# Kernel optimization log

Measured on AMD Instinct MI355X. Metric: run time of the kernel, lower is better.

The kernel has to match this reference:

```python
import jax, jax.numpy as jnp
import numpy as np

B, S, D, H = 2, 2048, 1024, 16
DK = D // H
SOFTCAP = 30.0


def setup_inputs() -> dict:
    key = jax.random.key(0)
    ks = jax.random.split(key, 6)
    inp = jax.random.normal(ks[0], (B, S, D), dtype=jnp.float32)
    count_bias = jax.random.normal(ks[1], (B, 1, S, S), dtype=jnp.float32) * 0.1
    # causal boolean mask: True = allowed
    causal = jnp.tril(jnp.ones((S, S), dtype=bool))
    attn_mask = jnp.broadcast_to(causal[None, None, :, :], (B, 1, S, S))
    scale = 0.02
    Wq = jax.random.normal(ks[2], (D, D), dtype=jnp.float32) * scale
    Wk = jax.random.normal(ks[3], (D, D), dtype=jnp.float32) * scale
    Wv = jax.random.normal(ks[4], (D, D), dtype=jnp.float32) * scale
    Wo = jax.random.normal(ks[5], (D, D), dtype=jnp.float32) * scale
    return {"inp": inp, "count_bias": count_bias, "attn_mask": attn_mask,
            "Wq": Wq, "Wk": Wk, "Wv": Wv, "Wo": Wo}


def reference(inp, count_bias, attn_mask, Wq, Wk, Wv, Wo):
    b = inp.shape[0]
    # nn.Linear: y = x @ W.T ; reshape to (B, H, S, DK)
    def proj(x, W):
        return jnp.einsum('bsd,ed->bse', x, W).reshape(b, -1, H, DK).transpose(0, 2, 1, 3)
    q = proj(inp, Wq)
    k = proj(inp, Wk)
    v = proj(inp, Wv)
    scale = 1.0 / np.sqrt(DK).astype(np.float32)
    scores = jnp.einsum('bhqd,bhkd->bhqk', q, k) * scale  # (B,H,S,S)
    scores = scores + count_bias  # broadcast over heads
    scores = jnp.tanh(scores / SOFTCAP) * SOFTCAP  # softcap > 0
    scores = jnp.where(attn_mask, scores, -jnp.inf)
    weights = jax.nn.softmax(scores, axis=-1)
    o = jnp.einsum('bhqk,bhkd->bhqd', weights, v)
    o = o.transpose(0, 2, 1, 3).reshape(b, -1, D)
    out = jnp.einsum('bsd,ed->bse', o, Wo)
    return out
```

## Files before the change

### kernel.cpp

```cpp
#include <hip/hip_runtime.h>
#include <hip/hip_bf16.h>

#define GK 1024

typedef __attribute__((ext_vector_type(8))) short bf16x8;
typedef __attribute__((ext_vector_type(4))) float f32x4;
typedef __attribute__((ext_vector_type(16))) float f32x16;
typedef __attribute__((ext_vector_type(4))) unsigned short ushort4v;

__device__ __forceinline__ f32x4 mfma16(bf16x8 a, bf16x8 b, f32x4 c) {
  return __builtin_amdgcn_mfma_f32_16x16x32_bf16(a, b, c, 0, 0, 0);
}
__device__ __forceinline__ f32x16 mfma32(bf16x8 a, bf16x8 b, f32x16 c) {
  return __builtin_amdgcn_mfma_f32_32x32x16_bf16(a, b, c, 0, 0, 0);
}

__device__ __forceinline__ unsigned short f2b(float f) {
  union { float f; unsigned int u; } x; x.f = f;
  return (unsigned short)((x.u + 0x7fffu + ((x.u >> 16) & 1u)) >> 16);
}

__device__ __forceinline__ unsigned int pk2(float lo, float hi) {
  float2 f; f.x = lo; f.y = hi;
  __hip_bfloat162 t = __float22bfloat162_rn(f);
  union { __hip_bfloat162 b; unsigned int u; } c; c.b = t;
  return c.u;
}

__device__ __forceinline__ float fexp2(float x) {
#if __has_builtin(__builtin_amdgcn_exp2f)
  return __builtin_amdgcn_exp2f(x);
#else
  return exp2f(x);
#endif
}
__device__ __forceinline__ float frcp(float x) {
#if __has_builtin(__builtin_amdgcn_rcpf)
  return __builtin_amdgcn_rcpf(x);
#else
  return 1.0f / x;
#endif
}

__device__ __forceinline__ void gl_lds16(const unsigned short* g, unsigned short* l) {
  __builtin_amdgcn_global_load_lds(
      (const __attribute__((address_space(1))) unsigned int*)g,
      (__attribute__((address_space(3))) unsigned int*)l, 16, 0, 0);
}

__global__ __launch_bounds__(256) void convert_kernel(
    const float* __restrict__ inp,
    const float* __restrict__ wq, const float* __restrict__ wk,
    const float* __restrict__ wv, const float* __restrict__ wo,
    unsigned short* __restrict__ Xb, unsigned short* __restrict__ Wcat)
{
  const size_t XN = (size_t)4194304;
  size_t i = ((size_t)blockIdx.x * 256 + threadIdx.x) * 4;
  const float* src; unsigned short* dst; size_t off;
  if (i < XN) {
    src = inp; dst = Xb; off = i;
  } else {
    size_t j = i - XN;
    int w = (int)(j >> 20);
    off = j & 1048575u;
    src = (w == 0) ? wq : (w == 1) ? wk : (w == 2) ? wv : wo;
    dst = Wcat + ((size_t)w << 20);
  }
  f32x4 v = *(const f32x4*)(src + off);
  ushort4v o;
#pragma unroll
  for (int t = 0; t < 4; ++t) o[t] = f2b(v[t]);
  *(ushort4v*)(dst + off) = o;
}

__device__ __forceinline__ void gemm_mainloop(
    const unsigned short* __restrict__ A, const unsigned short* __restrict__ Wt,
    int m0, int n0, int tid, unsigned short* As, unsigned short* Bs,
    f32x4 (&acc)[4][4])
{
  const int lane = tid & 63;
  const int wave = tid >> 6;
  const int wr = wave >> 1, wc = wave & 1;
  const int lq = lane & 15, g = lane >> 4;

  const int r_in = lane >> 2;
  const int c8 = (lane & 3) * 8;

  const unsigned short* Ap0 = A + (size_t)(m0 + wave * 32 + r_in) * GK + c8;
  const unsigned short* Ap1 = Ap0 + (size_t)16 * GK;
  const unsigned short* Wp0 = Wt + (size_t)(n0 + wave * 32 + r_in) * GK + c8;
  const unsigned short* Wp1 = Wp0 + (size_t)16 * GK;
  unsigned short* As0 = As + wave * 1024;
  unsigned short* Bs0 = Bs + wave * 1024;

  for (int kt = 0; kt < GK / 32; ++kt) {
    const int k0 = kt * 32;
    __syncthreads();
    gl_lds16(Ap0 + k0, As0);
    gl_lds16(Ap1 + k0, As0 + 512);
    gl_lds16(Wp0 + k0, Bs0);
    gl_lds16(Wp1 + k0, Bs0 + 512);
    __syncthreads();
    bf16x8 af[4], bfr[4];
#pragma unroll
    for (int i = 0; i < 4; ++i)
      af[i] = *(const bf16x8*)(As + (wr * 64 + i * 16 + lq) * 32 + g * 8);
#pragma unroll
    for (int j = 0; j < 4; ++j)
      bfr[j] = *(const bf16x8*)(Bs + (wc * 64 + j * 16 + lq) * 32 + g * 8);
#pragma unroll
    for (int i = 0; i < 4; ++i)
#pragma unroll
      for (int j = 0; j < 4; ++j)
        acc[i][j] = mfma16(af[i], bfr[j], acc[i][j]);
  }
}

__global__ __launch_bounds__(256) void gemm_qkv(
    const unsigned short* __restrict__ X, const unsigned short* __restrict__ Wcat,
    unsigned short* __restrict__ Qb, unsigned short* __restrict__ Kb,
    unsigned short* __restrict__ Vt)
{
  __shared__ unsigned short As[4096];
  __shared__ unsigned short Bs[4096];
  f32x4 acc[4][4];
#pragma unroll
  for (int i = 0; i < 4; ++i)
#pragma unroll
    for (int j = 0; j < 4; ++j) acc[i][j] = (f32x4){0.f, 0.f, 0.f, 0.f};

  const int z = blockIdx.z;
  const int m0 = blockIdx.x * 128, n0 = blockIdx.y * 128;
  gemm_mainloop(X, Wcat + ((size_t)z << 20), m0, n0, (int)threadIdx.x, As, Bs, acc);

  const int lane = threadIdx.x & 63;
  const int wave = threadIdx.x >> 6;
  const int wr = wave >> 1, wc = wave & 1, lq = lane & 15, g = lane >> 4;

  if (z < 2) {
    unsigned short* C = z ? Kb : Qb;
#pragma unroll
    for (int i = 0; i < 4; ++i)
#pragma unroll
      for (int j = 0; j < 4; ++j) {
        int col = n0 + wc * 64 + j * 16 + lq;
#pragma unroll
        for (int r = 0; r < 4; ++r) {
          int row = m0 + wr * 64 + i * 16 + g * 4 + r;
          C[(size_t)row * 1024 + col] = f2b(acc[i][j][r]);
        }
      }
  } else {
#pragma unroll
    for (int i = 0; i < 4; ++i)
#pragma unroll
      for (int j = 0; j < 4; ++j) {
        int col = n0 + wc * 64 + j * 16 + lq;
        int row0 = m0 + wr * 64 + i * 16 + g * 4;
        int b = row0 >> 11;
        int s = row0 & 2047;
        ushort4v pv;
#pragma unroll
        for (int r = 0; r < 4; ++r) pv[r] = f2b(acc[i][j][r]);
        *(ushort4v*)(Vt + (size_t)(b * 1024 + col) * 2048 + s) = pv;
      }
  }
}

__global__ __launch_bounds__(256) void gemm_out(
    const unsigned short* __restrict__ Ob, const unsigned short* __restrict__ Wo,
    float* __restrict__ out)
{
  __shared__ unsigned short As[4096];
  __shared__ unsigned short Bs[4096];
  f32x4 acc[4][4];
#pragma unroll
  for (int i = 0; i < 4; ++i)
#pragma unroll
    for (int j = 0; j < 4; ++j) acc[i][j] = (f32x4){0.f, 0.f, 0.f, 0.f};

  const int m0 = blockIdx.x * 128, n0 = blockIdx.y * 128;
  gemm_mainloop(Ob, Wo, m0, n0, (int)threadIdx.x, As, Bs, acc);

  const int lane = threadIdx.x & 63;
  const int wave = threadIdx.x >> 6;
  const int wr = wave >> 1, wc = wave & 1, lq = lane & 15, g = lane >> 4;
#pragma unroll
  for (int i = 0; i < 4; ++i)
#pragma unroll
    for (int j = 0; j < 4; ++j) {
      int col = n0 + wc * 64 + j * 16 + lq;
#pragma unroll
      for (int r = 0; r < 4; ++r) {
        int row = m0 + wr * 64 + i * 16 + g * 4 + r;
        out[(size_t)row * 1024 + col] = acc[i][j][r];
      }
    }
}

__device__ __forceinline__ void attn_chain(
    const bf16x8 (&qf)[4], const f32x4 (&bvs)[4],
    bf16x8 kf0, bf16x8 kf1, bf16x8 kf2, bf16x8 kf3,
    bf16x8 va00, bf16x8 va01, bf16x8 va10, bf16x8 va11,
    bool msk, int ql, int hi,
    f32x16& o0, f32x16& o1, float& pls)
{
  const float INV30 = 0.033333333333f;
  const float C3 = -0.333333333f, C5 = 0.133333333f;
  const float C1 = 43.28085122666891f;

  f32x16 st = {0.f,0.f,0.f,0.f,0.f,0.f,0.f,0.f,0.f,0.f,0.f,0.f,0.f,0.f,0.f,0.f};
  st = mfma32(kf0, qf[0], st);
  st = mfma32(kf1, qf[1], st);
  st = mfma32(kf2, qf[2], st);
  st = mfma32(kf3, qf[3], st);

  float p[16];
#pragma unroll
  for (int reg = 0; reg < 16; ++reg) {
    float v = fmaf(st[reg], 0.125f, bvs[reg >> 2][reg & 3]);
    float y = v * INV30;
    float y2 = y * y;
    float t = y * fmaf(y2, fmaf(y2, C5, C3), 1.0f);
    p[reg] = fexp2(fmaf(t, C1, -C1));
  }
  if (msk) {
#pragma unroll
    for (int reg = 0; reg < 16; ++reg) {
      int krow = (reg & 3) + 8 * (reg >> 2) + 4 * hi;
      p[reg] = (krow <= ql) ? p[reg] : 0.f;
    }
  }
  float a0 = (p[0] + p[1]) + (p[2] + p[3]);
  float a1 = (p[4] + p[5]) + (p[6] + p[7]);
  float a2 = (p[8] + p[9]) + (p[10] + p[11]);
  float a3 = (p[12] + p[13]) + (p[14] + p[15]);
  pls += (a0 + a1) + (a2 + a3);

  unsigned int wv[8];
#pragma unroll
  for (int j = 0; j < 8; ++j) wv[j] = pk2(p[2 * j], p[2 * j + 1]);
  unsigned int x0 = hi ? wv[0] : wv[2], x1 = hi ? wv[1] : wv[3];
  x0 = __shfl_xor(x0, 32); x1 = __shfl_xor(x1, 32);
  unsigned int y0 = hi ? wv[4] : wv[6], y1 = hi ? wv[5] : wv[7];
  y0 = __shfl_xor(y0, 32); y1 = __shfl_xor(y1, 32);
  union { unsigned int u[4]; bf16x8 v; } B0, B1;
  B0.u[0] = hi ? x0 : wv[0]; B0.u[1] = hi ? x1 : wv[1];
  B0.u[2] = hi ? wv[2] : x0; B0.u[3] = hi ? wv[3] : x1;
  B1.u[0] = hi ? y0 : wv[4]; B1.u[1] = hi ? y1 : wv[5];
  B1.u[2] = hi ? wv[6] : y0; B1.u[3] = hi ? wv[7] : y1;

  o0 = mfma32(va00, B0.v, o0);
  o0 = mfma32(va01, B1.v, o0);
  o1 = mfma32(va10, B0.v, o1);
  o1 = mfma32(va11, B1.v, o1);
}

__global__ __launch_bounds__(256, 2) void attn_fwd(
    const unsigned short* __restrict__ Qb, const unsigned short* __restrict__ Kb,
    const unsigned short* __restrict__ Vt, const float* __restrict__ bias,
    unsigned short* __restrict__ Ob)
{
  __shared__ float Obuf[2][2][64 * 33];
  __shared__ float lsumbuf[2][8 * 32];
  __shared__ float rowinv[2][32];

  const int lane = threadIdx.x & 63;
  const int w = threadIdx.x >> 6;
  const int bid = blockIdx.x;
  const int lwg = (bid & 7) * 128 + (bid >> 3);
  const int bh = lwg >> 5;
  const int qp = lwg & 31;
  const int b = bh >> 4, h = bh & 15;
  const int tA = qp, tB = 63 - qp;
  const int q0A = tA * 32, q0B = tB * 32;
  const int ql = lane & 31;
  const int hi = lane >> 5;

  const unsigned short* QpA = Qb + (size_t)(b * 2048 + q0A + ql) * 1024 + h * 64 + 8 * hi;
  const unsigned short* QpB = Qb + (size_t)(b * 2048 + q0B + ql) * 1024 + h * 64 + 8 * hi;
  bf16x8 qfA[4], qfB[4];
#pragma unroll
  for (int c = 0; c < 4; ++c) {
    qfA[c] = *(const bf16x8*)(QpA + 16 * c);
    qfB[c] = *(const bf16x8*)(QpB + 16 * c);
  }

  const unsigned short* Kp = Kb + (size_t)(b * 2048 + ql) * 1024 + h * 64 + 8 * hi;
  const unsigned short* Vp = Vt + (size_t)(bh * 64 + ql) * 2048 + 8 * hi;
  const float* BpA = bias + (size_t)b * 4194304 + (size_t)(q0A + ql) * 2048 + 4 * hi;
  const float* BpB = bias + (size_t)b * 4194304 + (size_t)(q0B + ql) * 2048 + 4 * hi;

  float plsA = 0.f, plsB = 0.f;
  f32x16 oA0 = {0.f,0.f,0.f,0.f,0.f,0.f,0.f,0.f,0.f,0.f,0.f,0.f,0.f,0.f,0.f,0.f};
  f32x16 oA1 = oA0, oB0 = oA0, oB1 = oA0;

  for (int kt = w; kt <= tB; kt += 4) {
    const int k0 = kt * 32;
    const unsigned short* kp = Kp + (size_t)k0 * 1024;
    bf16x8 kf0 = *(const bf16x8*)(kp);
    bf16x8 kf1 = *(const bf16x8*)(kp + 16);
    bf16x8 kf2 = *(const bf16x8*)(kp + 32);
    bf16x8 kf3 = *(const bf16x8*)(kp + 48);
    const unsigned short* vp = Vp + k0;
    bf16x8 va00 = *(const bf16x8*)(vp);
    bf16x8 va01 = *(const bf16x8*)(vp + 16);
    bf16x8 va10 = *(const bf16x8*)(vp + (size_t)32 * 2048);
    bf16x8 va11 = *(const bf16x8*)(vp + (size_t)32 * 2048 + 16);
    f32x4 bvsB[4];
#pragma unroll
    for (int j = 0; j < 4; ++j) bvsB[j] = *(const f32x4*)(BpB + k0 + 8 * j);
    if (kt <= tA) {
      f32x4 bvsA[4];
#pragma unroll
      for (int j = 0; j < 4; ++j) bvsA[j] = *(const f32x4*)(BpA + k0 + 8 * j);
      attn_chain(qfA, bvsA, kf0, kf1, kf2, kf3, va00, va01, va10, va11,
                 kt == tA, ql, hi, oA0, oA1, plsA);
    }
    attn_chain(qfB, bvsB, kf0, kf1, kf2, kf3, va00, va01, va10, va11,
               kt == tB, ql, hi, oB0, oB1, plsB);
  }

  lsumbuf[0][(w * 2 + hi) * 32 + ql] = plsA;
  lsumbuf[1][(w * 2 + hi) * 32 + ql] = plsB;
  if (w >= 2) {
#pragma unroll
    for (int reg = 0; reg < 16; ++reg) {
      int d0 = (reg & 3) + 8 * (reg >> 2) + 4 * hi;
      Obuf[0][w - 2][d0 * 33 + ql] = oA0[reg];
      Obuf[0][w - 2][(d0 + 32) * 33 + ql] = oA1[reg];
      Obuf[1][w - 2][d0 * 33 + ql] = oB0[reg];
      Obuf[1][w - 2][(d0 + 32) * 33 + ql] = oB1[reg];
    }
  }
  __syncthreads();
  if (w < 2) {
#pragma unroll
    for (int reg = 0; reg < 16; ++reg) {
      int d0 = (reg & 3) + 8 * (reg >> 2) + 4 * hi;
      Obuf[0][w][d0 * 33 + ql] += oA0[reg];
      Obuf[0][w][(d0 + 32) * 33 + ql] += oA1[reg];
      Obuf[1][w][d0 * 33 + ql] += oB0[reg];
      Obuf[1][w][(d0 + 32) * 33 + ql] += oB1[reg];
    }
  }
  __syncthreads();
  if (threadIdx.x < 64) {
    int t = threadIdx.x >> 5, q = threadIdx.x & 31;
    float s = 0.f;
#pragma unroll
    for (int j = 0; j < 8; ++j) s += lsumbuf[t][j * 32 + q];
    rowinv[t][q] = frcp(s);
  }
  __syncthreads();
#pragma unroll
  for (int it = 0; it < 16; ++it) {
    int i = it * 256 + (int)threadIdx.x;
    int t = i >> 11;
    int rem = i & 2047;
    int q = rem >> 6, d = rem & 63;
    float val = (Obuf[t][0][d * 33 + q] + Obuf[t][1][d * 33 + q]) * rowinv[t][q];
    int row = b * 2048 + (t ? q0B : q0A) + q;
    Ob[(size_t)row * 1024 + h * 64 + d] = f2b(val);
  }
}

extern "C" void kernel_launch(void* const* d_in, const int* in_sizes, int n_in,
                              void* d_out, int out_size, void* d_ws, size_t ws_size,
                              hipStream_t stream) {
  (void)in_sizes; (void)n_in; (void)out_size; (void)ws_size;
  const float* inp  = (const float*)d_in[0];
  const float* bias = (const float*)d_in[1];
  const float* wq = (const float*)d_in[3];
  const float* wk = (const float*)d_in[4];
  const float* wv = (const float*)d_in[5];
  const float* wo = (const float*)d_in[6];
  float* out = (float*)d_out;

  unsigned short* Xb   = (unsigned short*)d_ws;
  unsigned short* Wcat = Xb + 4194304;
  unsigned short* Qb   = Wcat + 4194304;
  unsigned short* Kb   = Qb + 4194304;
  unsigned short* Vt   = Kb + 4194304;
  unsigned short* Ob   = Vt + 4194304;

  convert_kernel<<<8192, 256, 0, stream>>>(inp, wq, wk, wv, wo, Xb, Wcat);
  gemm_qkv<<<dim3(32, 8, 3), dim3(256), 0, stream>>>(Xb, Wcat, Qb, Kb, Vt);
  attn_fwd<<<1024, 256, 0, stream>>>(Qb, Kb, Vt, bias, Ob);
  gemm_out<<<dim3(32, 8, 1), dim3(256), 0, stream>>>(Ob, Wcat + 3 * 1048576, out);
}
```

Baseline: 167.5 us.

## Pair adjacent query tiles per block and prefetch next K/V tile in registers

Each block now handles two adjacent 32-row query tiles instead of a mirrored pair (qp and 63-qp). Blocks are ordered longest-first so heavy work is scheduled early. Both tiles now share nearly all K/V tiles, and the loop register-prefetches the next K/V tile before running the current chain to hide global load latency. The trade-offs are uneven work across blocks, where the mirrored pairing previously balanced it, and extra register pressure from the double-buffered K/V fragments under the 2-blocks-per-CU launch bound.

```diff
diff --git a/kernel.cpp b/kernel.cpp
--- a/kernel.cpp
+++ b/kernel.cpp
@@ -256,6 +256,8 @@
   o1 = mfma32(va11, B1.v, o1);
 }
 
+struct KVregs { bf16x8 k0, k1, k2, k3, v0, v1, v2, v3; };
+
 __global__ __launch_bounds__(256, 2) void attn_fwd(
     const unsigned short* __restrict__ Qb, const unsigned short* __restrict__ Kb,
     const unsigned short* __restrict__ Vt, const float* __restrict__ bias,
@@ -268,57 +270,72 @@
   const int lane = threadIdx.x & 63;
   const int w = threadIdx.x >> 6;
   const int bid = blockIdx.x;
-  const int lwg = (bid & 7) * 128 + (bid >> 3);
-  const int bh = lwg >> 5;
-  const int qp = lwg & 31;
+  const int idx = bid >> 3;
+  const int bh = (bid & 7) * 4 + (idx >> 5);
+  const int qp = 31 - (idx & 31);
   const int b = bh >> 4, h = bh & 15;
-  const int tA = qp, tB = 63 - qp;
-  const int q0A = tA * 32, q0B = tB * 32;
+  const int tA = 2 * qp, tB = 2 * qp + 1;
+  const int q0A = tA * 32;
   const int ql = lane & 31;
   const int hi = lane >> 5;
 
   const unsigned short* QpA = Qb + (size_t)(b * 2048 + q0A + ql) * 1024 + h * 64 + 8 * hi;
-  const unsigned short* QpB = Qb + (size_t)(b * 2048 + q0B + ql) * 1024 + h * 64 + 8 * hi;
   bf16x8 qfA[4], qfB[4];
 #pragma unroll
   for (int c = 0; c < 4; ++c) {
     qfA[c] = *(const bf16x8*)(QpA + 16 * c);
-    qfB[c] = *(const bf16x8*)(QpB + 16 * c);
+    qfB[c] = *(const bf16x8*)(QpA + 32 * 1024 + 16 * c);
   }
 
   const unsigned short* Kp = Kb + (size_t)(b * 2048 + ql) * 1024 + h * 64 + 8 * hi;
   const unsigned short* Vp = Vt + (size_t)(bh * 64 + ql) * 2048 + 8 * hi;
   const float* BpA = bias + (size_t)b * 4194304 + (size_t)(q0A + ql) * 2048 + 4 * hi;
-  const float* BpB = bias + (size_t)b * 4194304 + (size_t)(q0B + ql) * 2048 + 4 * hi;
+  const float* BpB = BpA + (size_t)32 * 2048;
+
+  auto loadKV = [&](int k0) {
+    KVregs r;
+    const unsigned short* kp = Kp + (size_t)k0 * 1024;
+    r.k0 = *(const bf16x8*)(kp);
+    r.k1 = *(const bf16x8*)(kp + 16);
+    r.k2 = *(const bf16x8*)(kp + 32);
+    r.k3 = *(const bf16x8*)(kp + 48);
+    const unsigned short* vp = Vp + k0;
+    r.v0 = *(const bf16x8*)(vp);
+    r.v1 = *(const bf16x8*)(vp + 16);
+    r.v2 = *(const bf16x8*)(vp + (size_t)32 * 2048);
+    r.v3 = *(const bf16x8*)(vp + (size_t)32 * 2048 + 16);
+    return r;
+  };
 
   float plsA = 0.f, plsB = 0.f;
   f32x16 oA0 = {0.f,0.f,0.f,0.f,0.f,0.f,0.f,0.f,0.f,0.f,0.f,0.f,0.f,0.f,0.f,0.f};
   f32x16 oA1 = oA0, oB0 = oA0, oB1 = oA0;
 
-  for (int kt = w; kt <= tB; kt += 4) {
-    const int k0 = kt * 32;
-    const unsigned short* kp = Kp + (size_t)k0 * 1024;
-    bf16x8 kf0 = *(const bf16x8*)(kp);
-    bf16x8 kf1 = *(const bf16x8*)(kp + 16);
-    bf16x8 kf2 = *(const bf16x8*)(kp + 32);
-    bf16x8 kf3 = *(const bf16x8*)(kp + 48);
-    const unsigned short* vp = Vp + k0;
-    bf16x8 va00 = *(const bf16x8*)(vp);
-    bf16x8 va01 = *(const bf16x8*)(vp + 16);
-    bf16x8 va10 = *(const bf16x8*)(vp + (size_t)32 * 2048);
-    bf16x8 va11 = *(const bf16x8*)(vp + (size_t)32 * 2048 + 16);
+  KVregs cur, nxt;
+  int kt = w;
+  if (kt <= tA) cur = loadKV(kt * 32);
+  for (; kt <= tA; kt += 4) {
+    f32x4 bvsA[4], bvsB[4];
+#pragma unroll
+    for (int j = 0; j < 4; ++j) {
+      bvsA[j] = *(const f32x4*)(BpA + kt * 32 + 8 * j);
+      bvsB[j] = *(const f32x4*)(BpB + kt * 32 + 8 * j);
+    }
+    const bool pf = (kt + 4 <= tA);
+    if (pf) nxt = loadKV((kt + 4) * 32);
+    attn_chain(qfA, bvsA, cur.k0, cur.k1, cur.k2, cur.k3,
+               cur.v0, cur.v1, cur.v2, cur.v3, kt == tA, ql, hi, oA0, oA1, plsA);
+    attn_chain(qfB, bvsB, cur.k0, cur.k1, cur.k2, cur.k3,
+               cur.v0, cur.v1, cur.v2, cur.v3, false, ql, hi, oB0, oB1, plsB);
+    if (pf) cur = nxt;
+  }
+  if (kt == tB) {
+    cur = loadKV(kt * 32);
     f32x4 bvsB[4];
 #pragma unroll
-    for (int j = 0; j < 4; ++j) bvsB[j] = *(const f32x4*)(BpB + k0 + 8 * j);
-    if (kt <= tA) {
-      f32x4 bvsA[4];
-#pragma unroll
-      for (int j = 0; j < 4; ++j) bvsA[j] = *(const f32x4*)(BpA + k0 + 8 * j);
-      attn_chain(qfA, bvsA, kf0, kf1, kf2, kf3, va00, va01, va10, va11,
-                 kt == tA, ql, hi, oA0, oA1, plsA);
-    }
-    attn_chain(qfB, bvsB, kf0, kf1, kf2, kf3, va00, va01, va10, va11,
-               kt == tB, ql, hi, oB0, oB1, plsB);
+    for (int j = 0; j < 4; ++j) bvsB[j] = *(const f32x4*)(BpB + kt * 32 + 8 * j);
+    attn_chain(qfB, bvsB, cur.k0, cur.k1, cur.k2, cur.k3,
+               cur.v0, cur.v1, cur.v2, cur.v3, true, ql, hi, oB0, oB1, plsB);
   }
 
   lsumbuf[0][(w * 2 + hi) * 32 + ql] = plsA;
@@ -360,7 +377,7 @@
     int rem = i & 2047;
     int q = rem >> 6, d = rem & 63;
     float val = (Obuf[t][0][d * 33 + q] + Obuf[t][1][d * 33 + q]) * rowinv[t][q];
-    int row = b * 2048 + (t ? q0B : q0A) + q;
+    int row = b * 2048 + q0A + t * 32 + q;
     Ob[(size_t)row * 1024 + h * 64 + d] = f2b(val);
   }
 }
```

Result: slower. 175.1 us (+4.5%).

## Restructure attention to share K/V tiles across query-tile waves via LDS double buffering

Applied to the files above, without the earlier changes.

Each block now handles four consecutive 32-row query tiles, one per wave, instead of split-K over key tiles for a paired short/long query tile. K, V and bias tiles are staged into swizzled LDS with async global-to-LDS loads and double buffering, so K/V are fetched once per block and reused by all four waves. This removes the cross-wave output and row-sum reduction through LDS. In exchange, waves within a block do unequal causal work and sit idle at the per-iteration barriers, the grid shrinks to 512 blocks, and the launch bound no longer requests two blocks per CU.

```diff
diff --git a/kernel.cpp b/kernel.cpp
--- a/kernel.cpp
+++ b/kernel.cpp
@@ -42,7 +42,12 @@
 #endif
 }
 
-__device__ __forceinline__ void gl_lds16(const unsigned short* g, unsigned short* l) {
+__device__ __forceinline__ void gl_lds16(const unsigned short* g, void* l) {
+  __builtin_amdgcn_global_load_lds(
+      (const __attribute__((address_space(1))) unsigned int*)g,
+      (__attribute__((address_space(3))) unsigned int*)l, 16, 0, 0);
+}
+__device__ __forceinline__ void gl_lds16f(const float* g, void* l) {
   __builtin_amdgcn_global_load_lds(
       (const __attribute__((address_space(1))) unsigned int*)g,
       (__attribute__((address_space(3))) unsigned int*)l, 16, 0, 0);
@@ -198,170 +203,156 @@
     }
 }
 
-__device__ __forceinline__ void attn_chain(
-    const bf16x8 (&qf)[4], const f32x4 (&bvs)[4],
-    bf16x8 kf0, bf16x8 kf1, bf16x8 kf2, bf16x8 kf3,
-    bf16x8 va00, bf16x8 va01, bf16x8 va10, bf16x8 va11,
-    bool msk, int ql, int hi,
-    f32x16& o0, f32x16& o1, float& pls)
-{
+__global__ __launch_bounds__(256) void attn_fwd(
+    const unsigned short* __restrict__ Qb, const unsigned short* __restrict__ Kb,
+    const unsigned short* __restrict__ Vt, const float* __restrict__ bias,
+    unsigned short* __restrict__ Ob)
+{
+  __shared__ unsigned char lds[49152];
+
+  const int tid = (int)threadIdx.x;
+  const int lane = tid & 63;
+  const int w = tid >> 6;
+  const int bid = (int)blockIdx.x;
+  const int i = 15 - ((bid >> 3) & 15);
+  const int bh = (bid & 7) * 4 + (bid >> 7);
+  const int b = bh >> 4, h = bh & 15;
+  const int myt = 4 * i + w;
+  const int q0w = myt * 32;
+  const int ktmax = 4 * i + 3;
+  const int ql = lane & 31;
+  const int hi = lane >> 5;
+
+  const unsigned short* Qp = Qb + (size_t)(b * 2048 + q0w + ql) * 1024 + h * 64 + 8 * hi;
+  bf16x8 qf[4];
+#pragma unroll
+  for (int c = 0; c < 4; ++c) qf[c] = *(const bf16x8*)(Qp + 16 * c);
+
+  const int kr = 8 * w + (lane >> 3);
+  const int kcs = (lane & 7) ^ ((lane >> 3) & 7);
+  const unsigned short* Ksrc = Kb + (size_t)(b * 2048 + kr) * 1024 + h * 64 + kcs * 8;
+  const int vd = 16 * w + (lane >> 2);
+  const int vcs = (lane & 3) ^ ((lane >> 2) & 3);
+  const unsigned short* Vsrc = Vt + (size_t)(bh * 64 + vd) * 2048 + vcs * 8;
+  const int br = lane >> 3;
+  const int bcs = (lane & 7) ^ ((lane >> 3) & 7);
+  const float* Bsrc = bias + (size_t)b * 4194304 + (size_t)(q0w + br) * 2048 + bcs * 4;
+
+  unsigned char* const Kdst = lds + w * 1024;
+  unsigned char* const Vdst = lds + 8192 + w * 1024;
+  unsigned char* const Bdst = lds + 16384 + w * 4096;
+
   const float INV30 = 0.033333333333f;
   const float C3 = -0.333333333f, C5 = 0.133333333f;
   const float C1 = 43.28085122666891f;
 
-  f32x16 st = {0.f,0.f,0.f,0.f,0.f,0.f,0.f,0.f,0.f,0.f,0.f,0.f,0.f,0.f,0.f,0.f};
-  st = mfma32(kf0, qf[0], st);
-  st = mfma32(kf1, qf[1], st);
-  st = mfma32(kf2, qf[2], st);
-  st = mfma32(kf3, qf[3], st);
-
-  float p[16];
-#pragma unroll
-  for (int reg = 0; reg < 16; ++reg) {
-    float v = fmaf(st[reg], 0.125f, bvs[reg >> 2][reg & 3]);
-    float y = v * INV30;
-    float y2 = y * y;
-    float t = y * fmaf(y2, fmaf(y2, C5, C3), 1.0f);
-    p[reg] = fexp2(fmaf(t, C1, -C1));
-  }
-  if (msk) {
-#pragma unroll
-    for (int reg = 0; reg < 16; ++reg) {
-      int krow = (reg & 3) + 8 * (reg >> 2) + 4 * hi;
-      p[reg] = (krow <= ql) ? p[reg] : 0.f;
+  float pls = 0.f;
+  f32x16 oT0 = {0.f,0.f,0.f,0.f,0.f,0.f,0.f,0.f,0.f,0.f,0.f,0.f,0.f,0.f,0.f,0.f};
+  f32x16 oT1 = oT0;
+
+  auto stage = [&](int kt, int db) {
+    gl_lds16(Ksrc + (size_t)kt * 32768, Kdst + db * 4096);
+    gl_lds16(Vsrc + kt * 32, Vdst + db * 4096);
+    if (kt <= myt) {
+#pragma unroll
+      for (int j = 0; j < 4; ++j)
+        gl_lds16f(Bsrc + kt * 32 + j * 16384, Bdst + db * 16384 + j * 1024);
     }
-  }
-  float a0 = (p[0] + p[1]) + (p[2] + p[3]);
-  float a1 = (p[4] + p[5]) + (p[6] + p[7]);
-  float a2 = (p[8] + p[9]) + (p[10] + p[11]);
-  float a3 = (p[12] + p[13]) + (p[14] + p[15]);
-  pls += (a0 + a1) + (a2 + a3);
-
-  unsigned int wv[8];
-#pragma unroll
-  for (int j = 0; j < 8; ++j) wv[j] = pk2(p[2 * j], p[2 * j + 1]);
-  unsigned int x0 = hi ? wv[0] : wv[2], x1 = hi ? wv[1] : wv[3];
-  x0 = __shfl_xor(x0, 32); x1 = __shfl_xor(x1, 32);
-  unsigned int y0 = hi ? wv[4] : wv[6], y1 = hi ? wv[5] : wv[7];
-  y0 = __shfl_xor(y0, 32); y1 = __shfl_xor(y1, 32);
-  union { unsigned int u[4]; bf16x8 v; } B0, B1;
-  B0.u[0] = hi ? x0 : wv[0]; B0.u[1] = hi ? x1 : wv[1];
-  B0.u[2] = hi ? wv[2] : x0; B0.u[3] = hi ? wv[3] : x1;
-  B1.u[0] = hi ? y0 : wv[4]; B1.u[1] = hi ? y1 : wv[5];
-  B1.u[2] = hi ? wv[6] : y0; B1.u[3] = hi ? wv[7] : y1;
-
-  o0 = mfma32(va00, B0.v, o0);
-  o0 = mfma32(va01, B1.v, o0);
-  o1 = mfma32(va10, B0.v, o1);
-  o1 = mfma32(va11, B1.v, o1);
-}
-
-__global__ __launch_bounds__(256, 2) void attn_fwd(
-    const unsigned short* __restrict__ Qb, const unsigned short* __restrict__ Kb,
-    const unsigned short* __restrict__ Vt, const float* __restrict__ bias,
-    unsigned short* __restrict__ Ob)
-{
-  __shared__ float Obuf[2][2][64 * 33];
-  __shared__ float lsumbuf[2][8 * 32];
-  __shared__ float rowinv[2][32];
-
-  const int lane = threadIdx.x & 63;
-  const int w = threadIdx.x >> 6;
-  const int bid = blockIdx.x;
-  const int lwg = (bid & 7) * 128 + (bid >> 3);
-  const int bh = lwg >> 5;
-  const int qp = lwg & 31;
-  const int b = bh >> 4, h = bh & 15;
-  const int tA = qp, tB = 63 - qp;
-  const int q0A = tA * 32, q0B = tB * 32;
-  const int ql = lane & 31;
-  const int hi = lane >> 5;
-
-  const unsigned short* QpA = Qb + (size_t)(b * 2048 + q0A + ql) * 1024 + h * 64 + 8 * hi;
-  const unsigned short* QpB = Qb + (size_t)(b * 2048 + q0B + ql) * 1024 + h * 64 + 8 * hi;
-  bf16x8 qfA[4], qfB[4];
-#pragma unroll
-  for (int c = 0; c < 4; ++c) {
-    qfA[c] = *(const bf16x8*)(QpA + 16 * c);
-    qfB[c] = *(const bf16x8*)(QpB + 16 * c);
-  }
-
-  const unsigned short* Kp = Kb + (size_t)(b * 2048 + ql) * 1024 + h * 64 + 8 * hi;
-  const unsigned short* Vp = Vt + (size_t)(bh * 64 + ql) * 2048 + 8 * hi;
-  const float* BpA = bias + (size_t)b * 4194304 + (size_t)(q0A + ql) * 2048 + 4 * hi;
-  const float* BpB = bias + (size_t)b * 4194304 + (size_t)(q0B + ql) * 2048 + 4 * hi;
-
-  float plsA = 0.f, plsB = 0.f;
-  f32x16 oA0 = {0.f,0.f,0.f,0.f,0.f,0.f,0.f,0.f,0.f,0.f,0.f,0.f,0.f,0.f,0.f,0.f};
-  f32x16 oA1 = oA0, oB0 = oA0, oB1 = oA0;
-
-  for (int kt = w; kt <= tB; kt += 4) {
-    const int k0 = kt * 32;
-    const unsigned short* kp = Kp + (size_t)k0 * 1024;
-    bf16x8 kf0 = *(const bf16x8*)(kp);
-    bf16x8 kf1 = *(const bf16x8*)(kp + 16);
-    bf16x8 kf2 = *(const bf16x8*)(kp + 32);
-    bf16x8 kf3 = *(const bf16x8*)(kp + 48);
-    const unsigned short* vp = Vp + k0;
-    bf16x8 va00 = *(const bf16x8*)(vp);
-    bf16x8 va01 = *(const bf16x8*)(vp + 16);
-    bf16x8 va10 = *(const bf16x8*)(vp + (size_t)32 * 2048);
-    bf16x8 va11 = *(const bf16x8*)(vp + (size_t)32 * 2048 + 16);
-    f32x4 bvsB[4];
-#pragma unroll
-    for (int j = 0; j < 4; ++j) bvsB[j] = *(const f32x4*)(BpB + k0 + 8 * j);
-    if (kt <= tA) {
-      f32x4 bvsA[4];
-#pragma unroll
-      for (int j = 0; j < 4; ++j) bvsA[j] = *(const f32x4*)(BpA + k0 + 8 * j);
-      attn_chain(qfA, bvsA, kf0, kf1, kf2, kf3, va00, va01, va10, va11,
-                 kt == tA, ql, hi, oA0, oA1, plsA);
+  };
+
+  stage(0, 0);
+  __syncthreads();
+
+  int cur = 0;
+  for (int kt = 0; kt <= ktmax; ++kt) {
+    if (kt < ktmax) stage(kt + 1, cur ^ 1);
+
+    if (kt <= myt) {
+      const unsigned char* Ksh = lds + cur * 4096;
+      const unsigned char* Vsh = lds + 8192 + cur * 4096;
+      const unsigned char* Bsh = lds + 16384 + cur * 16384 + w * 4096;
+      const int q7 = (ql & 7) << 4;
+      const int q3 = (ql & 3) << 4;
+
+      bf16x8 kf[4];
+#pragma unroll
+      for (int c = 0; c < 4; ++c)
+        kf[c] = *(const bf16x8*)(Ksh + ql * 128 + (((hi + 2 * c) << 4) ^ q7));
+      f32x4 bvs[4];
+#pragma unroll
+      for (int j = 0; j < 4; ++j)
+        bvs[j] = *(const f32x4*)(Bsh + ql * 128 + (((hi + 2 * j) << 4) ^ q7));
+      bf16x8 va00 = *(const bf16x8*)(Vsh + ql * 64 + ((hi << 4) ^ q3));
+      bf16x8 va01 = *(const bf16x8*)(Vsh + ql * 64 + (((hi + 2) << 4) ^ q3));
+      bf16x8 va10 = *(const bf16x8*)(Vsh + (32 + ql) * 64 + ((hi << 4) ^ q3));
+      bf16x8 va11 = *(const bf16x8*)(Vsh + (32 + ql) * 64 + (((hi + 2) << 4) ^ q3));
+
+      f32x16 st = {0.f,0.f,0.f,0.f,0.f,0.f,0.f,0.f,0.f,0.f,0.f,0.f,0.f,0.f,0.f,0.f};
+      st = mfma32(kf[0], qf[0], st);
+      st = mfma32(kf[1], qf[1], st);
+      st = mfma32(kf[2], qf[2], st);
+      st = mfma32(kf[3], qf[3], st);
+
+      float p[16];
+#pragma unroll
+      for (int reg = 0; reg < 16; ++reg) {
+        float v = fmaf(st[reg], 0.125f, bvs[reg >> 2][reg & 3]);
+        float y = v * INV30;
+        float y2 = y * y;
+        float t = y * fmaf(y2, fmaf(y2, C5, C3), 1.0f);
+        p[reg] = fexp2(fmaf(t, C1, -C1));
+      }
+      if (kt == myt) {
+#pragma unroll
+        for (int reg = 0; reg < 16; ++reg) {
+          int krow = (reg & 3) + 8 * (reg >> 2) + 4 * hi;
+          p[reg] = (krow <= ql) ? p[reg] : 0.f;
+        }
+      }
+      float a0 = (p[0] + p[1]) + (p[2] + p[3]);
+      float a1 = (p[4] + p[5]) + (p[6] + p[7]);
+      float a2 = (p[8] + p[9]) + (p[10] + p[11]);
+      float a3 = (p[12] + p[13]) + (p[14] + p[15]);
+      pls += (a0 + a1) + (a2 + a3);
+
+      unsigned int wv[8];
+#pragma unroll
+      for (int j = 0; j < 8; ++j) wv[j] = pk2(p[2 * j], p[2 * j + 1]);
+      unsigned int x0 = hi ? wv[0] : wv[2], x1 = hi ? wv[1] : wv[3];
+      x0 = __shfl_xor(x0, 32); x1 = __shfl_xor(x1, 32);
+      unsigned int y0 = hi ? wv[4] : wv[6], y1 = hi ? wv[5] : wv[7];
+      y0 = __shfl_xor(y0, 32); y1 = __shfl_xor(y1, 32);
+      union { unsigned int u[4]; bf16x8 v; } B0, B1;
+      B0.u[0] = hi ? x0 : wv[0]; B0.u[1] = hi ? x1 : wv[1];
+      B0.u[2] = hi ? wv[2] : x0; B0.u[3] = hi ? wv[3] : x1;
+      B1.u[0] = hi ? y0 : wv[4]; B1.u[1] = hi ? y1 : wv[5];
+      B1.u[2] = hi ? wv[6] : y0; B1.u[3] = hi ? wv[7] : y1;
+
+      oT0 = mfma32(va00, B0.v, oT0);
+      oT0 = mfma32(va01, B1.v, oT0);
+      oT1 = mfma32(va10, B0.v, oT1);
+      oT1 = mfma32(va11, B1.v, oT1);
     }
-    attn_chain(qfB, bvsB, kf0, kf1, kf2, kf3, va00, va01, va10, va11,
-               kt == tB, ql, hi, oB0, oB1, plsB);
-  }
-
-  lsumbuf[0][(w * 2 + hi) * 32 + ql] = plsA;
-  lsumbuf[1][(w * 2 + hi) * 32 + ql] = plsB;
-  if (w >= 2) {
-#pragma unroll
-    for (int reg = 0; reg < 16; ++reg) {
-      int d0 = (reg & 3) + 8 * (reg >> 2) + 4 * hi;
-      Obuf[0][w - 2][d0 * 33 + ql] = oA0[reg];
-      Obuf[0][w - 2][(d0 + 32) * 33 + ql] = oA1[reg];
-      Obuf[1][w - 2][d0 * 33 + ql] = oB0[reg];
-      Obuf[1][w - 2][(d0 + 32) * 33 + ql] = oB1[reg];
-    }
-  }
-  __syncthreads();
-  if (w < 2) {
-#pragma unroll
-    for (int reg = 0; reg < 16; ++reg) {
-      int d0 = (reg & 3) + 8 * (reg >> 2) + 4 * hi;
-      Obuf[0][w][d0 * 33 + ql] += oA0[reg];
-      Obuf[0][w][(d0 + 32) * 33 + ql] += oA1[reg];
-      Obuf[1][w][d0 * 33 + ql] += oB0[reg];
-      Obuf[1][w][(d0 + 32) * 33 + ql] += oB1[reg];
-    }
-  }
-  __syncthreads();
-  if (threadIdx.x < 64) {
-    int t = threadIdx.x >> 5, q = threadIdx.x & 31;
-    float s = 0.f;
-#pragma unroll
-    for (int j = 0; j < 8; ++j) s += lsumbuf[t][j * 32 + q];
-    rowinv[t][q] = frcp(s);
-  }
-  __syncthreads();
-#pragma unroll
-  for (int it = 0; it < 16; ++it) {
-    int i = it * 256 + (int)threadIdx.x;
-    int t = i >> 11;
-    int rem = i & 2047;
-    int q = rem >> 6, d = rem & 63;
-    float val = (Obuf[t][0][d * 33 + q] + Obuf[t][1][d * 33 + q]) * rowinv[t][q];
-    int row = b * 2048 + (t ? q0B : q0A) + q;
-    Ob[(size_t)row * 1024 + h * 64 + d] = f2b(val);
+
+    __syncthreads();
+    cur ^= 1;
+  }
+
+  pls += __shfl_xor(pls, 32);
+  float rl = frcp(pls);
+  unsigned short* T = (unsigned short*)(lds + 16384 + w * 4096);
+#pragma unroll
+  for (int r = 0; r < 16; r += 2) {
+    int d0 = (r & 3) + 8 * (r >> 2) + 4 * hi;
+    *(unsigned int*)(T + ql * 64 + d0) = pk2(oT0[r] * rl, oT0[r + 1] * rl);
+    *(unsigned int*)(T + ql * 64 + 32 + d0) = pk2(oT1[r] * rl, oT1[r + 1] * rl);
+  }
+#pragma unroll
+  for (int j = 0; j < 4; ++j) {
+    int idx = j * 64 + lane;
+    int q = idx >> 3, c = idx & 7;
+    bf16x8 val = *(const bf16x8*)(T + q * 64 + c * 8);
+    *(bf16x8*)(Ob + (size_t)(b * 2048 + q0w + q) * 1024 + h * 64 + c * 8) = val;
   }
 }
 
@@ -386,6 +377,6 @@
 
   convert_kernel<<<8192, 256, 0, stream>>>(inp, wq, wk, wv, wo, Xb, Wcat);
   gemm_qkv<<<dim3(32, 8, 3), dim3(256), 0, stream>>>(Xb, Wcat, Qb, Kb, Vt);
-  attn_fwd<<<1024, 256, 0, stream>>>(Qb, Kb, Vt, bias, Ob);
+  attn_fwd<<<512, 256, 0, stream>>>(Qb, Kb, Vt, bias, Ob);
   gemm_out<<<dim3(32, 8, 1), dim3(256), 0, stream>>>(Ob, Wcat + 3 * 1048576, out);
 }
```

After: 176.7 us. 1.05x slower.

## Double-buffer K/V tiles in LDS via async global_load_lds with swizzle

Applied to the files above, without the earlier changes.

Each wave now prefetches its next K and V tiles into its own double-buffered LDS region with direct global-to-LDS loads, using an XOR swizzle to avoid bank conflicts. It then reads MFMA fragments from LDS instead of issuing strided global loads right before use. This is meant to hide global load latency behind the attention math. The block-to-(batch,head,query-pair) mapping is also changed, and a 64KB LDS buffer is shared with the reduction scratch, which may lower occupancy below the launch-bound target of 2 blocks.

```diff
diff --git a/kernel.cpp b/kernel.cpp
--- a/kernel.cpp
+++ b/kernel.cpp
@@ -42,7 +42,7 @@
 #endif
 }
 
-__device__ __forceinline__ void gl_lds16(const unsigned short* g, unsigned short* l) {
+__device__ __forceinline__ void gl_lds16(const void* g, void* l) {
   __builtin_amdgcn_global_load_lds(
       (const __attribute__((address_space(1))) unsigned int*)g,
       (__attribute__((address_space(3))) unsigned int*)l, 16, 0, 0);
@@ -261,16 +261,14 @@
     const unsigned short* __restrict__ Vt, const float* __restrict__ bias,
     unsigned short* __restrict__ Ob)
 {
-  __shared__ float Obuf[2][2][64 * 33];
-  __shared__ float lsumbuf[2][8 * 32];
-  __shared__ float rowinv[2][32];
-
-  const int lane = threadIdx.x & 63;
-  const int w = threadIdx.x >> 6;
-  const int bid = blockIdx.x;
-  const int lwg = (bid & 7) * 128 + (bid >> 3);
-  const int bh = lwg >> 5;
-  const int qp = lwg & 31;
+  __shared__ __attribute__((aligned(16))) unsigned char lds[65536];
+
+  const int tid = (int)threadIdx.x;
+  const int lane = tid & 63;
+  const int w = tid >> 6;
+  const int bid = (int)blockIdx.x;
+  const int bh = (bid & 7) * 4 + ((bid >> 3) & 3);
+  const int qp = bid >> 5;
   const int b = bh >> 4, h = bh & 15;
   const int tA = qp, tB = 63 - qp;
   const int q0A = tA * 32, q0B = tB * 32;
@@ -286,8 +284,13 @@
     qfB[c] = *(const bf16x8*)(QpB + 16 * c);
   }
 
-  const unsigned short* Kp = Kb + (size_t)(b * 2048 + ql) * 1024 + h * 64 + 8 * hi;
-  const unsigned short* Vp = Vt + (size_t)(bh * 64 + ql) * 2048 + 8 * hi;
+  const unsigned short* KsrcL = Kb + (size_t)(b * 2048 + (lane >> 3)) * 1024
+                                + h * 64 + (((lane & 7) ^ ((lane >> 3) & 7)) << 3);
+  const unsigned short* VsrcL = Vt + (size_t)(bh * 64 + (lane >> 2)) * 2048
+                                + (((lane & 3) ^ ((lane >> 2) & 3)) << 3);
+  unsigned char* const KdstW = lds + w * 16384;
+  unsigned char* const VdstW = lds + w * 16384 + 8192;
+
   const float* BpA = bias + (size_t)b * 4194304 + (size_t)(q0A + ql) * 2048 + 4 * hi;
   const float* BpB = bias + (size_t)b * 4194304 + (size_t)(q0B + ql) * 2048 + 4 * hi;
 
@@ -295,71 +298,101 @@
   f32x16 oA0 = {0.f,0.f,0.f,0.f,0.f,0.f,0.f,0.f,0.f,0.f,0.f,0.f,0.f,0.f,0.f,0.f};
   f32x16 oA1 = oA0, oB0 = oA0, oB1 = oA0;
 
-  for (int kt = w; kt <= tB; kt += 4) {
-    const int k0 = kt * 32;
-    const unsigned short* kp = Kp + (size_t)k0 * 1024;
-    bf16x8 kf0 = *(const bf16x8*)(kp);
-    bf16x8 kf1 = *(const bf16x8*)(kp + 16);
-    bf16x8 kf2 = *(const bf16x8*)(kp + 32);
-    bf16x8 kf3 = *(const bf16x8*)(kp + 48);
-    const unsigned short* vp = Vp + k0;
-    bf16x8 va00 = *(const bf16x8*)(vp);
-    bf16x8 va01 = *(const bf16x8*)(vp + 16);
-    bf16x8 va10 = *(const bf16x8*)(vp + (size_t)32 * 2048);
-    bf16x8 va11 = *(const bf16x8*)(vp + (size_t)32 * 2048 + 16);
-    f32x4 bvsB[4];
-#pragma unroll
-    for (int j = 0; j < 4; ++j) bvsB[j] = *(const f32x4*)(BpB + k0 + 8 * j);
-    if (kt <= tA) {
-      f32x4 bvsA[4];
-#pragma unroll
-      for (int j = 0; j < 4; ++j) bvsA[j] = *(const f32x4*)(BpA + k0 + 8 * j);
-      attn_chain(qfA, bvsA, kf0, kf1, kf2, kf3, va00, va01, va10, va11,
-                 kt == tA, ql, hi, oA0, oA1, plsA);
+  auto stageKV = [&](int kt, int db) {
+#pragma unroll
+    for (int j = 0; j < 4; ++j)
+      gl_lds16(KsrcL + (size_t)kt * 32768 + j * 8192, KdstW + db * 4096 + j * 1024);
+#pragma unroll
+    for (int j = 0; j < 4; ++j)
+      gl_lds16(VsrcL + (size_t)j * 32768 + kt * 32, VdstW + db * 4096 + j * 1024);
+  };
+
+  stageKV(w, 0);
+  int db = 0;
+  for (int kt0 = 0; kt0 <= tB; kt0 += 4) {
+    const int mykt = kt0 + w;
+    asm volatile("s_waitcnt vmcnt(0)" ::: "memory");
+    __builtin_amdgcn_sched_barrier(0);
+    if (mykt + 4 <= tB) stageKV(mykt + 4, db ^ 1);
+    __builtin_amdgcn_sched_barrier(0);
+
+    if (mykt <= tB) {
+      const unsigned char* Ksh = lds + w * 16384 + db * 4096;
+      const unsigned char* Vsh = lds + w * 16384 + 8192 + db * 4096;
+      bf16x8 kf[4];
+#pragma unroll
+      for (int c = 0; c < 4; ++c)
+        kf[c] = *(const bf16x8*)(Ksh + ql * 128 + (((hi + 2 * c) ^ (ql & 7)) << 4));
+      const int vb = ((ql >> 4) << 10) + ((ql & 15) << 6);
+      bf16x8 va00 = *(const bf16x8*)(Vsh + vb + (((hi) ^ (ql & 3)) << 4));
+      bf16x8 va01 = *(const bf16x8*)(Vsh + vb + (((hi + 2) ^ (ql & 3)) << 4));
+      bf16x8 va10 = *(const bf16x8*)(Vsh + 2048 + vb + (((hi) ^ (ql & 3)) << 4));
+      bf16x8 va11 = *(const bf16x8*)(Vsh + 2048 + vb + (((hi + 2) ^ (ql & 3)) << 4));
+
+      f32x4 bvsB[4];
+#pragma unroll
+      for (int j = 0; j < 4; ++j) bvsB[j] = *(const f32x4*)(BpB + mykt * 32 + 8 * j);
+      attn_chain(qfB, bvsB, kf[0], kf[1], kf[2], kf[3], va00, va01, va10, va11,
+                 mykt == tB, ql, hi, oB0, oB1, plsB);
+      if (mykt <= tA) {
+        f32x4 bvsA[4];
+#pragma unroll
+        for (int j = 0; j < 4; ++j) bvsA[j] = *(const f32x4*)(BpA + mykt * 32 + 8 * j);
+        attn_chain(qfA, bvsA, kf[0], kf[1], kf[2], kf[3], va00, va01, va10, va11,
+                   mykt == tA, ql, hi, oA0, oA1, plsA);
+      }
     }
-    attn_chain(qfB, bvsB, kf0, kf1, kf2, kf3, va00, va01, va10, va11,
-               kt == tB, ql, hi, oB0, oB1, plsB);
-  }
-
-  lsumbuf[0][(w * 2 + hi) * 32 + ql] = plsA;
-  lsumbuf[1][(w * 2 + hi) * 32 + ql] = plsB;
+    db ^= 1;
+  }
+
+  __syncthreads();
+  float* ldsF = (float*)lds;
+  float* lsumbuf = ldsF + 8448;
+  float* rowinv = ldsF + 8960;
+  lsumbuf[(w * 2 + hi) * 32 + ql] = plsA;
+  lsumbuf[256 + (w * 2 + hi) * 32 + ql] = plsB;
   if (w >= 2) {
+    float* OA = ldsF + (w - 2) * 2112;
+    float* OB = ldsF + (2 + (w - 2)) * 2112;
 #pragma unroll
     for (int reg = 0; reg < 16; ++reg) {
       int d0 = (reg & 3) + 8 * (reg >> 2) + 4 * hi;
-      Obuf[0][w - 2][d0 * 33 + ql] = oA0[reg];
-      Obuf[0][w - 2][(d0 + 32) * 33 + ql] = oA1[reg];
-      Obuf[1][w - 2][d0 * 33 + ql] = oB0[reg];
-      Obuf[1][w - 2][(d0 + 32) * 33 + ql] = oB1[reg];
+      OA[d0 * 33 + ql] = oA0[reg];
+      OA[(d0 + 32) * 33 + ql] = oA1[reg];
+      OB[d0 * 33 + ql] = oB0[reg];
+      OB[(d0 + 32) * 33 + ql] = oB1[reg];
     }
   }
   __syncthreads();
   if (w < 2) {
+    float* OA = ldsF + w * 2112;
+    float* OB = ldsF + (2 + w) * 2112;
 #pragma unroll
     for (int reg = 0; reg < 16; ++reg) {
       int d0 = (reg & 3) + 8 * (reg >> 2) + 4 * hi;
-      Obuf[0][w][d0 * 33 + ql] += oA0[reg];
-      Obuf[0][w][(d0 + 32) * 33 + ql] += oA1[reg];
-      Obuf[1][w][d0 * 33 + ql] += oB0[reg];
-      Obuf[1][w][(d0 + 32) * 33 + ql] += oB1[reg];
+      OA[d0 * 33 + ql] += oA0[reg];
+      OA[(d0 + 32) * 33 + ql] += oA1[reg];
+      OB[d0 * 33 + ql] += oB0[reg];
+      OB[(d0 + 32) * 33 + ql] += oB1[reg];
     }
   }
   __syncthreads();
-  if (threadIdx.x < 64) {
-    int t = threadIdx.x >> 5, q = threadIdx.x & 31;
+  if (tid < 64) {
+    int t = tid >> 5, q = tid & 31;
     float s = 0.f;
 #pragma unroll
-    for (int j = 0; j < 8; ++j) s += lsumbuf[t][j * 32 + q];
-    rowinv[t][q] = frcp(s);
+    for (int j = 0; j < 8; ++j) s += lsumbuf[t * 256 + j * 32 + q];
+    rowinv[t * 32 + q] = frcp(s);
   }
   __syncthreads();
 #pragma unroll
   for (int it = 0; it < 16; ++it) {
-    int i = it * 256 + (int)threadIdx.x;
+    int i = it * 256 + tid;
     int t = i >> 11;
     int rem = i & 2047;
     int q = rem >> 6, d = rem & 63;
-    float val = (Obuf[t][0][d * 33 + q] + Obuf[t][1][d * 33 + q]) * rowinv[t][q];
+    float val = (ldsF[t * 4224 + d * 33 + q] + ldsF[t * 4224 + 2112 + d * 33 + q])
+                * rowinv[t * 32 + q];
     int row = b * 2048 + (t ? q0B : q0A) + q;
     Ob[(size_t)row * 1024 + h * 64 + d] = f2b(val);
   }
```

Result: faster. 140.5 us (-16.1%).
